# Kernel optimization log

Measured on AMD Instinct MI355X. Metric: run time of the kernel, lower is better.

Reference implementation:

```python
import jax, jax.numpy as jnp
import numpy as np

B, S = 2, 1024
ENC_IN, MARK_IN = 21, 4
PRED_LEN, C_OUT = 96, 21
E = 512                 # embedding_dim
INNER = 2 * E           # proj_factor=2.0 (library default; Model does not pass it)
NH = 8                  # mLSTM heads
DH = INNER // NH        # 128
K = 4                   # causal conv1d kernel
BS = 4                  # qkv_proj_blocksize
NHP = INNER // BS       # 256 block-diagonal proj heads
NB = 4                  # num_blocks
EPS = 1e-5


def setup_inputs() -> dict:
    key = jax.random.key(0)
    ks = jax.random.split(key, 24)
    it = iter(range(24))
    def n(shape, s=0.02):
        return jax.random.normal(ks[next(it)], shape, jnp.float32) * s
    return {
        "x_enc": n((B, S, ENC_IN), 1.0),
        "x_mark_enc": n((B, S, MARK_IN), 1.0),
        "x_dec": n((B, PRED_LEN, ENC_IN), 1.0),
        "x_mark_dec": n((B, PRED_LEN, MARK_IN), 1.0),
        "emb_W": n((ENC_IN + MARK_IN, E), 0.05),
        "emb_b": jnp.zeros((E,), jnp.float32),
        "ln_w": jnp.ones((NB, E), jnp.float32),
        "up_W": n((NB, E, 2 * INNER)),
        "conv_W": n((NB, INNER, K), 0.1),
        "conv_b": jnp.zeros((NB, INNER), jnp.float32),
        "q_W": n((NB, NHP, BS, BS), 0.1),
        "k_W": n((NB, NHP, BS, BS), 0.1),
        "v_W": n((NB, NHP, BS, BS), 0.1),
        "ig_W": n((NB, 3 * INNER, NH)),
        "ig_b": jnp.zeros((NB, NH), jnp.float32),
        "fg_W": n((NB, 3 * INNER, NH)),
        "fg_b": jnp.tile(jnp.linspace(3.0, 6.0, NH, dtype=jnp.float32), (NB, 1)),
        "skip": jnp.ones((NB, INNER), jnp.float32),
        "onorm_w": jnp.ones((NB, INNER), jnp.float32),
        "down_W": n((NB, INNER, E)),
        "post_ln_w": jnp.ones((E,), jnp.float32),
        "head_W": n((E, C_OUT), 0.05),
        "head_b": jnp.zeros((C_OUT,), jnp.float32),
    }


def _ln(x, w):
    mu = jnp.mean(x, -1, keepdims=True)
    var = jnp.var(x, -1, keepdims=True)
    return (x - mu) * jax.lax.rsqrt(var + EPS) * w


def _headwise(x, w):
    # block-diagonal LinearHeadwiseExpand: (B,S,INNER) with (NHP,BS,BS) blocks
    xh = x.reshape(x.shape[0], x.shape[1], NHP, BS)
    return jnp.einsum('bshd,hod->bsho', xh, w).reshape(x.shape)


def _block(x, lw, uW, cW, cb, qW, kW, vW, igW, igb, fgW, fgb, sk, ow, dW):
    xn = _ln(x, lw)
    up = xn @ uW                                  # (B,S,2*INNER)
    xm, z = up[..., :INNER], up[..., INNER:]
    # causal depthwise conv1d + SiLU
    xc = jax.lax.conv_general_dilated(
        xm.transpose(0, 2, 1), cW[:, None, :], (1,), [(K - 1, 0)],
        feature_group_count=INNER,
        dimension_numbers=('NCH', 'OIH', 'NCH')).transpose(0, 2, 1) + cb
    xc = jax.nn.silu(xc)
    q = _headwise(xc, qW)
    k = _headwise(xc, kW)
    v = _headwise(xm, vW)
    qkv = jnp.concatenate([q, k, v], -1)          # (B,S,3*INNER)
    ig = (qkv @ igW + igb).transpose(0, 2, 1)     # (B,NH,S)
    fg = (qkv @ fgW + fgb).transpose(0, 2, 1)
    qh = q.reshape(B, S, NH, DH).transpose(0, 2, 1, 3)
    kh = k.reshape(B, S, NH, DH).transpose(0, 2, 1, 3)
    vh = v.reshape(B, S, NH, DH).transpose(0, 2, 1, 3)
    # parallel stabilized mLSTM (exp-gated linear attention)
    log_f = jax.nn.log_sigmoid(fg)
    cs = jnp.cumsum(log_f, -1)                    # (B,NH,S)
    Mmat = cs[..., :, None] - cs[..., None, :]    # (B,NH,S,S) cumulative decay
    tri = jnp.tril(jnp.ones((S, S), bool))
    logD = jnp.where(tri, Mmat + ig[..., None, :], -jnp.inf)
    m = jnp.max(logD, -1, keepdims=True)          # row-wise stabilizer
    D = jnp.exp(logD - m)
    qk = jnp.einsum('bnsd,bntd->bnst', qh, kh) / (DH ** 0.5)
    C = qk * D
    norm = jnp.maximum(jnp.abs(jnp.sum(C, -1, keepdims=True)), jnp.exp(-m))
    h = jnp.einsum('bnst,bntd->bnsd', C / (norm + 1e-6), vh)
    # multi-head layernorm (groupnorm over DH per head), weight, no bias
    hn = (h - jnp.mean(h, -1, keepdims=True)) * jax.lax.rsqrt(jnp.var(h, -1, keepdims=True) + EPS)
    hn = hn.transpose(0, 2, 1, 3).reshape(B, S, INNER) * ow
    hs = (hn + sk * xc) * jax.nn.silu(z)          # learnable skip + output gate
    return x + hs @ dW                            # residual


def reference(x_enc, x_mark_enc, x_dec, x_mark_dec, emb_W, emb_b, ln_w, up_W,
              conv_W, conv_b, q_W, k_W, v_W, ig_W, ig_b, fg_W, fg_b, skip,
              onorm_w, down_W, post_ln_w, head_W, head_b):
    x = jnp.concatenate([x_enc, x_mark_enc], -1) @ emb_W + emb_b
    for i in range(NB):
        x = _block(x, ln_w[i], up_W[i], conv_W[i], conv_b[i], q_W[i], k_W[i],
                   v_W[i], ig_W[i], ig_b[i], fg_W[i], fg_b[i], skip[i],
                   onorm_w[i], down_W[i])
    x = _ln(x, post_ln_w)
    return x[:, -PRED_LEN:, :] @ head_W + head_b
```

## Files before the change

### kernel.cpp

```cpp
#include <hip/hip_runtime.h>
#include <hip/hip_bf16.h>

#define S_LEN 1024
#define E_DIM 512
#define INNER_D 1024
#define NHEAD 8
#define DHEAD 128

typedef unsigned short u16;
typedef unsigned int u32;
typedef __attribute__((ext_vector_type(8))) short short8;
typedef __attribute__((ext_vector_type(4))) float f32x4;

union S8 { short8 v; u16 u[8]; uint4 q; };

__device__ __forceinline__ u16 f2bf(float f) {
  u32 u = __float_as_uint(f);
  u32 r = u + 0x7FFFu + ((u >> 16) & 1u);
  return (u16)(r >> 16);
}
__device__ __forceinline__ float bf2f(u16 u) { return __uint_as_float(((u32)u) << 16); }

__device__ __forceinline__ void gload16(const u16* g, u16* l) {
  __builtin_amdgcn_global_load_lds((const __attribute__((address_space(1))) void*)g,
                                   (__attribute__((address_space(3))) void*)l, 16, 0, 0);
}

__global__ __launch_bounds__(128) void embed_kernel(
    const float* __restrict__ xe, const float* __restrict__ xm,
    const float* __restrict__ W, const float* __restrict__ bias,
    float* __restrict__ x)
{
  int row = blockIdx.x;
  int tid = threadIdx.x;
  __shared__ float in_s[25];
  if (tid < 21) in_s[tid] = xe[row * 21 + tid];
  else if (tid < 25) in_s[tid] = xm[row * 4 + tid - 21];
  __syncthreads();
#pragma unroll
  for (int rep = 0; rep < 4; rep++) {
    int e = tid + rep * 128;
    float acc = bias[e];
#pragma unroll
    for (int i = 0; i < 25; i++) acc += in_s[i] * W[i * E_DIM + e];
    x[(size_t)row * E_DIM + e] = acc;
  }
}

__global__ __launch_bounds__(256) void ln_kernel(
    const float* __restrict__ x, const float* __restrict__ w, u16* __restrict__ out)
{
  int row = blockIdx.x, tid = threadIdx.x;
  const float* xr = x + (size_t)row * E_DIM;
  float2 v = *(const float2*)(xr + tid * 2);
  float s = v.x + v.y, q = v.x * v.x + v.y * v.y;
#pragma unroll
  for (int off = 32; off; off >>= 1) { s += __shfl_xor(s, off); q += __shfl_xor(q, off); }
  __shared__ float ssum[4], ssq[4];
  int wv = tid >> 6;
  if ((tid & 63) == 0) { ssum[wv] = s; ssq[wv] = q; }
  __syncthreads();
  s = ssum[0] + ssum[1] + ssum[2] + ssum[3];
  q = ssq[0] + ssq[1] + ssq[2] + ssq[3];
  float mu = s * (1.f / E_DIM);
  float var = q * (1.f / E_DIM) - mu * mu;
  float rs = rsqrtf(var + 1e-5f);
  int e = tid * 2;
  ushort2 o;
  o.x = f2bf((v.x - mu) * rs * w[e]);
  o.y = f2bf((v.y - mu) * rs * w[e + 1]);
  *(ushort2*)(out + (size_t)row * E_DIM + e) = o;
}

__global__ __launch_bounds__(256) void lnhead_kernel(
    const float* __restrict__ x, const float* __restrict__ w,
    const float* __restrict__ hW, const float* __restrict__ hb,
    float* __restrict__ out)
{
  int ridx = blockIdx.x;
  int b = ridx / 96, r = ridx % 96;
  int row = b * S_LEN + (S_LEN - 96) + r;
  int tid = threadIdx.x;
  const float* xr = x + (size_t)row * E_DIM;
  float2 v = *(const float2*)(xr + tid * 2);
  float s = v.x + v.y, q = v.x * v.x + v.y * v.y;
#pragma unroll
  for (int off = 32; off; off >>= 1) { s += __shfl_xor(s, off); q += __shfl_xor(q, off); }
  __shared__ float ssum[4], ssq[4];
  __shared__ float lnv[512];
  __shared__ float part[8][32];
  int wv = tid >> 6;
  if ((tid & 63) == 0) { ssum[wv] = s; ssq[wv] = q; }
  __syncthreads();
  s = ssum[0] + ssum[1] + ssum[2] + ssum[3];
  q = ssq[0] + ssq[1] + ssq[2] + ssq[3];
  float mu = s * (1.f / E_DIM);
  float var = q * (1.f / E_DIM) - mu * mu;
  float rs = rsqrtf(var + 1e-5f);
  int e = tid * 2;
  lnv[e]     = (v.x - mu) * rs * w[e];
  lnv[e + 1] = (v.y - mu) * rs * w[e + 1];
  __syncthreads();
  int n = tid & 31, sl = tid >> 5;
  float p = 0.f;
  if (n < 21) {
#pragma unroll 8
    for (int kk = 0; kk < 64; kk++)
      p += lnv[sl * 64 + kk] * hW[(sl * 64 + kk) * 21 + n];
  }
  part[sl][n] = p;
  __syncthreads();
  if (tid < 21) {
    float acc = hb[tid];
#pragma unroll
    for (int j = 0; j < 8; j++) acc += part[j][tid];
    out[ridx * 21 + tid] = acc;
  }
}

__global__ __launch_bounds__(256) void transpose_bf16_all_kernel(
    const float* __restrict__ in0, u16* __restrict__ out0, int K, int N)
{
  __shared__ u16 T[64][72];
  int L = blockIdx.z;
  const float* in = in0 + (size_t)L * K * N;
  u16* out = out0 + (size_t)L * N * K;
  int k0 = blockIdx.x * 64, n0 = blockIdx.y * 64;
  int t = threadIdx.x;
  int kr = t >> 2, nseg = (t & 3) * 16;
  const float* src = in + (size_t)(k0 + kr) * N + n0 + nseg;
#pragma unroll
  for (int j = 0; j < 16; j++) T[kr][nseg + j] = f2bf(src[j]);
  __syncthreads();
  int nr = t >> 2, kseg = (t & 3) * 16;
  u32 u[8];
#pragma unroll
  for (int rr = 0; rr < 8; rr++) {
    u32 lo = T[kseg + 2 * rr][nr];
    u32 hi = T[kseg + 2 * rr + 1][nr];
    u[rr] = lo | (hi << 16);
  }
  u16* dst = out + (size_t)(n0 + nr) * K + k0 + kseg;
  uint4 w0 = {u[0], u[1], u[2], u[3]};
  uint4 w1 = {u[4], u[5], u[6], u[7]};
  *(uint4*)dst = w0;
  *(uint4*)(dst + 8) = w1;
}

__global__ __launch_bounds__(256) void vtrans_kernel(
    const u16* __restrict__ v, u16* __restrict__ vt)
{
  __shared__ u16 T[64][72];
  int r0 = blockIdx.x * 64;
  int d0 = blockIdx.y * 64;
  int t = threadIdx.x;
  int sr = t >> 2, dseg = (t & 3) * 16;
  const u16* src = v + (size_t)(r0 + sr) * INNER_D + d0 + dseg;
  S8 a0, a1;
  a0.q = *(const uint4*)src;
  a1.q = *(const uint4*)(src + 8);
#pragma unroll
  for (int j = 0; j < 8; j++) { T[sr][dseg + j] = a0.u[j]; T[sr][dseg + 8 + j] = a1.u[j]; }
  __syncthreads();
  int dr = t >> 2, sseg = (t & 3) * 16;
  u32 u[8];
#pragma unroll
  for (int rr = 0; rr < 8; rr++) {
    u32 lo = T[sseg + 2 * rr][dr];
    u32 hi = T[sseg + 2 * rr + 1][dr];
    u[rr] = lo | (hi << 16);
  }
  int b = r0 >> 10;
  u16* dst = vt + ((size_t)b * INNER_D + d0 + dr) * S_LEN + (r0 & (S_LEN - 1)) + sseg;
  uint4 w0 = {u[0], u[1], u[2], u[3]};
  uint4 w1 = {u[4], u[5], u[6], u[7]};
  *(uint4*)dst = w0;
  *(uint4*)(dst + 8) = w1;
}

__global__ __launch_bounds__(256) void gates_w_transpose_kernel(
    const float* __restrict__ igW, const float* __restrict__ fgW,
    u16* __restrict__ hi, u16* __restrict__ lo)
{
  int L = blockIdx.z;
  int n = blockIdx.y;
  int k = blockIdx.x * 256 + threadIdx.x;
  const float* W = ((n < 8) ? igW : fgW) + (size_t)L * 24576;
  float v = W[(size_t)k * 8 + (n & 7)];
  u16 h = f2bf(v);
  u16 l = f2bf(v - bf2f(h));
  size_t o = ((size_t)L * 16 + n) * 3072 + k;
  hi[o] = h;
  lo[o] = l;
}

__global__ __launch_bounds__(256) void gemm_bf16_split64(
    const u16* __restrict__ A, const u16* __restrict__ Bt,
    float* __restrict__ C0, u16* __restrict__ C1,
    int M, int N, int K, int split_col, int ldc)
{
  __shared__ u16 As0[128 * 32], As1[128 * 32];
  __shared__ u16 Bs0[128 * 32], Bs1[128 * 32];
  const int tid = threadIdx.x;
  const int row0 = blockIdx.y * 128, col0 = blockIdx.x * 128;
  const int wave = tid >> 6, lane = tid & 63;
  const int wr = wave >> 1, wc = wave & 1;
  const int lm = lane & 15, lq = lane >> 4;
  const int lr4 = lane >> 2;
  const int cg4 = (lane & 3) ^ (lr4 & 3);
  f32x4 acc[4][4] = {};
  const u16* Abase = A + (size_t)(row0 + lr4) * K + cg4 * 8;
  const u16* Bbase = Bt + (size_t)(col0 + lr4) * K + cg4 * 8;
  const int key = lm & 3;

#define STG_UP(AS, BS, K0) do { \
  _Pragma("unroll") for (int i = 0; i < 2; i++) \
    gload16(Abase + (size_t)((wave * 2 + i) * 16) * K + (K0), &AS[(wave * 2 + i) * 512]); \
  _Pragma("unroll") for (int i = 0; i < 2; i++) \
    gload16(Bbase + (size_t)((wave * 2 + i) * 16) * K + (K0), &BS[(wave * 2 + i) * 512]); \
} while (0)

#define CMP_UP(AS, BS) do { \
  short8 af[4], bfv[4]; \
  _Pragma("unroll") for (int i = 0; i < 4; i++) \
    af[i] = *(const short8*)&AS[(wr * 64 + i * 16 + lm) * 32 + ((lq ^ key) * 8)]; \
  _Pragma("unroll") for (int j = 0; j < 4; j++) \
    bfv[j] = *(const short8*)&BS[(wc * 64 + j * 16 + lm) * 32 + ((lq ^ key) * 8)]; \
  _Pragma("unroll") for (int i = 0; i < 4; i++) \
    _Pragma("unroll") for (int j = 0; j < 4; j++) \
      acc[i][j] = __builtin_amdgcn_mfma_f32_16x16x32_bf16(af[i], bfv[j], acc[i][j], 0, 0, 0); \
} while (0)

  STG_UP(As0, Bs0, 0);
  asm volatile("" ::: "memory");
  STG_UP(As1, Bs1, 32);
#pragma unroll
  for (int t = 0; t < 16; t++) {
    if (t < 15) asm volatile("s_waitcnt vmcnt(4)" ::: "memory");
    else        asm volatile("s_waitcnt vmcnt(0)" ::: "memory");
    __builtin_amdgcn_sched_barrier(0);
    __builtin_amdgcn_s_barrier();
    if (t & 1) CMP_UP(As1, Bs1); else CMP_UP(As0, Bs0);
    __builtin_amdgcn_s_barrier();
    if (t + 2 < 16) {
      if (t & 1) STG_UP(As1, Bs1, (t + 2) * 32);
      else       STG_UP(As0, Bs0, (t + 2) * 32);
    }
  }
#undef STG_UP
#undef CMP_UP

  const bool toC1 = (col0 >= split_col);
#pragma unroll
  for (int i = 0; i < 4; i++) {
#pragma unroll
    for (int j = 0; j < 4; j++) {
      int col = col0 - (toC1 ? split_col : 0) + wc * 64 + j * 16 + lm;
#pragma unroll
      for (int r = 0; r < 4; r++) {
        int row = row0 + wr * 64 + i * 16 + lq * 4 + r;
        if (toC1) C1[(size_t)row * ldc + col] = f2bf(acc[i][j][r]);
        else C0[(size_t)row * ldc + col] = acc[i][j][r];
      }
    }
  }
}

__global__ __launch_bounds__(256) void gemm_bf16_32(
    const u16* __restrict__ A, const u16* __restrict__ Bt,
    float* __restrict__ C, int M, int N, int K, int ldc)
{
  __shared__ u16 As0[64 * 64], As1[64 * 64];
  __shared__ u16 Bs0[64 * 64], Bs1[64 * 64];
  const int tid = threadIdx.x;
  const int row0 = blockIdx.y * 64, col0 = blockIdx.x * 64;
  const int wave = tid >> 6, lane = tid & 63;
  const int wr = wave >> 1, wc = wave & 1;
  const int lm = lane & 15, lq = lane >> 4;
  const int lr = lane >> 3;
  const int cg = (lane & 7) ^ lr;
  f32x4 acc[2][2] = {};
  const u16* Abase = A + (size_t)(row0 + lr) * K + cg * 8;
  const u16* Bbase = Bt + (size_t)(col0 + lr) * K + cg * 8;
  const int key = lm & 7;

#define STAGE_DN(AS, BS, K0) do { \
  _Pragma("unroll") for (int i = 0; i < 2; i++) \
    gload16(Abase + (size_t)((wave * 2 + i) * 8) * K + (K0), &AS[(wave * 2 + i) * 512]); \
  _Pragma("unroll") for (int j = 0; j < 2; j++) \
    gload16(Bbase + (size_t)((wave * 2 + j) * 8) * K + (K0), &BS[(wave * 2 + j) * 512]); \
} while (0)

#define COMPUTE_DN(AS, BS) do { \
  short8 af[2][2], bfv[2][2]; \
  _Pragma("unroll") for (int kc = 0; kc < 2; kc++) { \
    _Pragma("unroll") for (int i = 0; i < 2; i++) \
      af[kc][i] = *(const short8*)&AS[(wr * 32 + i * 16 + lm) * 64 + (((kc * 4 + lq) ^ key) * 8)]; \
    _Pragma("unroll") for (int j = 0; j < 2; j++) \
      bfv[kc][j] = *(const short8*)&BS[(wc * 32 + j * 16 + lm) * 64 + (((kc * 4 + lq) ^ key) * 8)]; \
  } \
  _Pragma("unroll") for (int kc = 0; kc < 2; kc++) \
    _Pragma("unroll") for (int i = 0; i < 2; i++) \
      _Pragma("unroll") for (int j = 0; j < 2; j++) \
        acc[i][j] = __builtin_amdgcn_mfma_f32_16x16x32_bf16(af[kc][i], bfv[kc][j], acc[i][j], 0, 0, 0); \
} while (0)

  STAGE_DN(As0, Bs0, 0);
  asm volatile("" ::: "memory");
  STAGE_DN(As1, Bs1, 64);
#pragma unroll
  for (int t = 0; t < 16; t++) {
    if (t < 15) asm volatile("s_waitcnt vmcnt(4)" ::: "memory");
    else        asm volatile("s_waitcnt vmcnt(0)" ::: "memory");
    __builtin_amdgcn_sched_barrier(0);
    __builtin_amdgcn_s_barrier();
    if (t & 1) COMPUTE_DN(As1, Bs1); else COMPUTE_DN(As0, Bs0);
    __builtin_amdgcn_s_barrier();
    if (t + 2 < 16) {
      if (t & 1) STAGE_DN(As1, Bs1, (t + 2) * 64);
      else       STAGE_DN(As0, Bs0, (t + 2) * 64);
    }
  }
#undef STAGE_DN
#undef COMPUTE_DN

#pragma unroll
  for (int i = 0; i < 2; i++) {
#pragma unroll
    for (int j = 0; j < 2; j++) {
      int col = col0 + wc * 32 + j * 16 + lm;
#pragma unroll
      for (int r = 0; r < 4; r++) {
        int row = row0 + wr * 32 + i * 16 + lq * 4 + r;
        C[(size_t)row * ldc + col] += acc[i][j][r];
      }
    }
  }
}

__global__ __launch_bounds__(256) void convqkv_kernel(
    const float* __restrict__ xm,
    const float* __restrict__ cw, const float* __restrict__ cb,
    const float* __restrict__ qw, const float* __restrict__ kw, const float* __restrict__ vw,
    float* __restrict__ xc, u16* __restrict__ q, u16* __restrict__ k, u16* __restrict__ v)
{
  int r0 = blockIdx.x * 8;
  int s0 = r0 & (S_LEN - 1);
  int g = threadIdx.x;
  int c0 = g * 4;
  const float* base = xm + (size_t)r0 * INNER_D + c0;

  float4 xv[11];
#pragma unroll
  for (int j = 0; j < 11; j++) {
    int ts = s0 - 3 + j;
    float4 t = {0.f, 0.f, 0.f, 0.f};
    if (ts >= 0) t = *(const float4*)(base + (ptrdiff_t)(j - 3) * INNER_D);
    xv[j] = t;
  }
  float cwv[4][4];
#pragma unroll
  for (int c = 0; c < 4; c++)
#pragma unroll
    for (int kk = 0; kk < 4; kk++) cwv[c][kk] = cw[(c0 + c) * 4 + kk];
  float cbv[4] = {cb[c0], cb[c0 + 1], cb[c0 + 2], cb[c0 + 3]};
  const float* qg = qw + g * 16;
  const float* kg = kw + g * 16;
  const float* vg = vw + g * 16;
  float qwv[16], kwv[16], vwv[16];
#pragma unroll
  for (int i = 0; i < 16; i++) { qwv[i] = qg[i]; kwv[i] = kg[i]; vwv[i] = vg[i]; }

#pragma unroll
  for (int i = 0; i < 8; i++) {
    float a0 = cbv[0], a1 = cbv[1], a2 = cbv[2], a3 = cbv[3];
#pragma unroll
    for (int kk = 0; kk < 4; kk++) {
      float4 xvv = xv[i + kk];
      a0 += xvv.x * cwv[0][kk];
      a1 += xvv.y * cwv[1][kk];
      a2 += xvv.z * cwv[2][kk];
      a3 += xvv.w * cwv[3][kk];
    }
    a0 = a0 / (1.f + __expf(-a0));
    a1 = a1 / (1.f + __expf(-a1));
    a2 = a2 / (1.f + __expf(-a2));
    a3 = a3 / (1.f + __expf(-a3));
    float4 accv = {a0, a1, a2, a3};
    *(float4*)(xc + (size_t)(r0 + i) * INNER_D + c0) = accv;

    float xcv[4] = {a0, a1, a2, a3};
    float xmv[4] = {xv[i + 3].x, xv[i + 3].y, xv[i + 3].z, xv[i + 3].w};
    ushort4 qs, ks, vs;
    u16* qp = (u16*)&qs; u16* kp = (u16*)&ks; u16* vp = (u16*)&vs;
#pragma unroll
    for (int o = 0; o < 4; o++) {
      float aq = 0.f, ak = 0.f, av = 0.f;
#pragma unroll
      for (int d = 0; d < 4; d++) {
        aq += xcv[d] * qwv[o * 4 + d];
        ak += xcv[d] * kwv[o * 4 + d];
        av += xmv[d] * vwv[o * 4 + d];
      }
      qp[o] = f2bf(aq); kp[o] = f2bf(ak); vp[o] = f2bf(av);
    }
    size_t off = (size_t)(r0 + i) * INNER_D + c0;
    *(ushort4*)(q + off) = qs;
    *(ushort4*)(k + off) = ks;
    *(ushort4*)(v + off) = vs;
  }
}

__global__ __launch_bounds__(256) void gates_mfma_kernel(
    const u16* __restrict__ q, const u16* __restrict__ k, const u16* __restrict__ v,
    const u16* __restrict__ whi, const u16* __restrict__ wlo,
    const float* __restrict__ igb, const float* __restrict__ fgb,
    float* __restrict__ ig, float* __restrict__ fg)
{
  const int blk = blockIdx.x;
  const int tid = threadIdx.x;
  const int wave = tid >> 6, lane = tid & 63;
  const int lm = lane & 15, lq = lane >> 4;
  const int grow = blk * 16 + lm;
  const u16* parts[3] = {q, k, v};
  f32x4 acc = {};
#pragma unroll 4
  for (int kc = 0; kc < 24; kc++) {
    int k0 = wave * 768 + kc * 32;
    int part = k0 >> 10;
    int idx = (k0 & 1023) + lq * 8;
    S8 a, bh_, bl_;
    a.q = *(const uint4*)(parts[part] + (size_t)grow * INNER_D + idx);
    bh_.q = *(const uint4*)(whi + (size_t)lm * 3072 + k0 + lq * 8);
    bl_.q = *(const uint4*)(wlo + (size_t)lm * 3072 + k0 + lq * 8);
    __builtin_amdgcn_s_setprio(1);
    acc = __builtin_amdgcn_mfma_f32_16x16x32_bf16(a.v, bh_.v, acc, 0, 0, 0);
    acc = __builtin_amdgcn_mfma_f32_16x16x32_bf16(a.v, bl_.v, acc, 0, 0, 0);
    __builtin_amdgcn_s_setprio(0);
  }
  __shared__ float red[4][16][17];
#pragma unroll
  for (int r = 0; r < 4; r++) red[wave][lq * 4 + r][lm] = acc[r];
  __syncthreads();
  if (wave == 0) {
#pragma unroll
    for (int r = 0; r < 4; r++) {
      int row = lq * 4 + r;
      float sum = red[0][row][lm] + red[1][row][lm] + red[2][row][lm] + red[3][row][lm];
      int growr = blk * 16 + row;
      int b = growr >> 10, s = growr & (S_LEN - 1);
      if (lm < 8) ig[((size_t)(b * NHEAD + lm) << 10) + s] = sum + igb[lm];
      else        fg[((size_t)(b * NHEAD + (lm - 8)) << 10) + s] = sum + fgb[lm - 8];
    }
  }
}

__global__ __launch_bounds__(1024) void scan_kernel(
    const float* __restrict__ ig, const float* __restrict__ fg,
    float* __restrict__ a, float* __restrict__ rm, float* __restrict__ enm)
{
  int bh = blockIdx.x;
  int t = threadIdx.x;
  int lane = t & 63, wv = t >> 6;
  __shared__ float sw[16];
  size_t o = ((size_t)bh << 10) + t;
  float f = fg[o];
  float lf = (f >= 0.f) ? -log1pf(__expf(-f)) : f - log1pf(__expf(f));
  float v = lf;
#pragma unroll
  for (int off = 1; off < 64; off <<= 1) {
    float u = __shfl_up(v, off);
    if (lane >= off) v += u;
  }
  if (lane == 63) sw[wv] = v;
  __syncthreads();
  float pre = 0.f;
  for (int w = 0; w < wv; w++) pre += sw[w];
  float cs = v + pre;
  float av = ig[o] - cs;
  a[o] = av;
  float m = av;
#pragma unroll
  for (int off = 1; off < 64; off <<= 1) {
    float u = __shfl_up(m, off);
    if (lane >= off) m = fmaxf(m, u);
  }
  __syncthreads();
  if (lane == 63) sw[wv] = m;
  __syncthreads();
  float pm = -3.4e38f;
  for (int w = 0; w < wv; w++) pm = fmaxf(pm, sw[w]);
  float rmx = fmaxf(m, pm);
  rm[o] = rmx;
  enm[o] = __expf(-(cs + rmx));
}

__device__ __constant__ int c_qt[24] = {7,15,14,15, 6,13,14,12,13, 5,11,12,10,11, 4, 9,10, 8, 9, 3, 8, 2, 1, 0};
__device__ __constant__ int c_k0[24] = {0, 0, 7, 8, 0, 0, 0, 6, 7, 0, 0, 0, 5, 6, 0, 0, 0, 4, 5, 0, 0, 0, 0, 0};
__device__ __constant__ int c_k1[24] = {8, 8,15,16, 7, 7, 7,13,14, 6, 6, 6,11,12, 5, 5, 5, 9,10, 4, 4, 3, 2, 1};
__device__ __constant__ int c_md[24] = {0, 1, 2, 2, 0, 1, 1, 2, 2, 0, 1, 1, 2, 2, 0, 1, 1, 2, 2, 0, 1, 0, 0, 0};

__global__ __launch_bounds__(256) void attn_mfma_kernel(
    const u16* __restrict__ qhg, const u16* __restrict__ khg, const u16* __restrict__ vtg,
    const float* __restrict__ a_arr, const float* __restrict__ rm_arr, const float* __restrict__ enm_arr,
    const float* __restrict__ xc, const u16* __restrict__ zh,
    const float* __restrict__ skip, const float* __restrict__ onw,
    u16* __restrict__ hs, float* __restrict__ hpart, float* __restrict__ scpart)
{
  const int bh = blockIdx.x;
  const int job = blockIdx.y;
  const int qt = c_qt[job], k0t = c_k0[job], k1t = c_k1[job], mode = c_md[job];
  const int b = bh >> 3, h = bh & 7;
  const int s0 = qt * 64;
  const int tid = threadIdx.x;
  const int wave = tid >> 6, lane = tid & 63;
  const int lm = lane & 15, lq = lane >> 4;
  const size_t rowbase = (size_t)b * S_LEN;
  const int c0 = h * DHEAD;

  __shared__ u16 Ks0[64 * 128], Ks1[64 * 128];
  __shared__ u16 Vt0[128 * 64], Vt1[128 * 64];
  __shared__ u16 Ws[64 * 72];

  short8 aq[4];
  {
    const u16* qp = qhg + (rowbase + s0 + wave * 16 + lm) * INNER_D + c0 + lq * 8;
#pragma unroll
    for (int kc = 0; kc < 4; kc++) {
      S8 tmp; tmp.q = *(const uint4*)(qp + kc * 32);
      aq[kc] = tmp.v;
    }
  }
  float rmv[4];
#pragma unroll
  for (int r = 0; r < 4; r++)
    rmv[r] = rm_arr[(size_t)bh * S_LEN + s0 + wave * 16 + lq * 4 + r];

  f32x4 accH[8] = {};
  float sc_acc[4] = {0.f, 0.f, 0.f, 0.f};
  const float scale = 0.08838834764831845f;
  const int lr16 = lane >> 4;
  const int ls16 = lane & 15;
  const int lr8 = lane >> 3;
  const int cgv = (lane & 7) ^ lr8;
  const u16* vtbase = vtg + ((size_t)b * INNER_D + c0) * S_LEN;

  float ae0[4], ae1[4];

#define PREF(KS, VS, AE, T0) do { \
  _Pragma("unroll") for (int j = 0; j < 4; j++) { \
    int rK = (wave * 4 + j) * 4 + lr16; \
    int cgk = ls16 ^ (rK & 7); \
    gload16(khg + (rowbase + (T0) + rK) * INNER_D + c0 + cgk * 8, &KS[(wave * 4 + j) * 512]); \
  } \
  _Pragma("unroll") for (int j = 0; j < 4; j++) { \
    int rV = (wave * 4 + j) * 8 + lr8; \
    gload16(vtbase + (size_t)rV * S_LEN + (T0) + cgv * 8, &VS[(wave * 4 + j) * 512]); \
  } \
  _Pragma("unroll") for (int cb = 0; cb < 4; cb++) \
    AE[cb] = a_arr[(size_t)bh * S_LEN + (T0) + cb * 16 + lm]; \
} while (0)

#define QK_STEP(KS, PACC) do { \
  __builtin_amdgcn_s_setprio(1); \
  _Pragma("unroll") for (int kc = 0; kc < 4; kc++) \
    _Pragma("unroll") for (int cb = 0; cb < 4; cb++) { \
      short8 bk = *(const short8*)&KS[(cb * 16 + lm) * 128 + (((kc * 4 + lq) ^ (lm & 7)) * 8)]; \
      PACC[cb] = __builtin_amdgcn_mfma_f32_16x16x32_bf16(aq[kc], bk, PACC[cb], 0, 0, 0); \
    } \
  __builtin_amdgcn_s_setprio(0); \
} while (0)

#define W_PV(AE, VT, T0, PACC) do { \
  float wpart[4] = {0.f, 0.f, 0.f, 0.f}; \
  _Pragma("unroll") for (int cb = 0; cb < 4; cb++) { \
    int colg = (T0) + cb * 16 + lm; \
    float ea = AE[cb]; \
    _Pragma("unroll") for (int r = 0; r < 4; r++) { \
      int rowg = s0 + wave * 16 + lq * 4 + r; \
      float wv = PACC[cb][r] * scale * __expf(ea - rmv[r]); \
      if (colg > rowg) wv = 0.f; \
      wpart[r] += wv; \
      Ws[(wave * 16 + lq * 4 + r) * 72 + cb * 16 + lm] = f2bf(wv); \
    } \
  } \
  _Pragma("unroll") for (int r = 0; r < 4; r++) { \
    float sr = wpart[r]; \
    sr += __shfl_xor(sr, 1); sr += __shfl_xor(sr, 2); \
    sr += __shfl_xor(sr, 4); sr += __shfl_xor(sr, 8); \
    sc_acc[r] += sr; \
  } \
  __builtin_amdgcn_s_setprio(1); \
  _Pragma("unroll") for (int kc = 0; kc < 2; kc++) { \
    short8 aw = *(const short8*)&Ws[(wave * 16 + lm) * 72 + kc * 32 + lq * 8]; \
    _Pragma("unroll") for (int nb = 0; nb < 8; nb++) { \
      short8 bv = *(const short8*)&VT[(nb * 16 + lm) * 64 + (((kc * 4 + lq) ^ (lm & 7)) * 8)]; \
      accH[nb] = __builtin_amdgcn_mfma_f32_16x16x32_bf16(aw, bv, accH[nb], 0, 0, 0); \
    } \
  } \
  __builtin_amdgcn_s_setprio(0); \
} while (0)

  int kt = k0t;
  PREF(Ks0, Vt0, ae0, kt * 64);
  asm volatile("" ::: "memory");
  if (kt + 1 < k1t) PREF(Ks1, Vt1, ae1, (kt + 1) * 64);

  while (true) {
    {
      if (kt + 1 < k1t) asm volatile("s_waitcnt vmcnt(12)" ::: "memory");
      else              asm volatile("s_waitcnt vmcnt(0)" ::: "memory");
      __builtin_amdgcn_sched_barrier(0);
      __builtin_amdgcn_s_barrier();
      f32x4 pacc[4] = {};
      QK_STEP(Ks0, pacc);
      W_PV(ae0, Vt0, kt * 64, pacc);
      __builtin_amdgcn_s_barrier();
      if (kt + 2 < k1t) PREF(Ks0, Vt0, ae0, (kt + 2) * 64);
      kt++;
      if (kt >= k1t) break;
    }
    {
      if (kt + 1 < k1t) asm volatile("s_waitcnt vmcnt(12)" ::: "memory");
      else              asm volatile("s_waitcnt vmcnt(0)" ::: "memory");
      __builtin_amdgcn_sched_barrier(0);
      __builtin_amdgcn_s_barrier();
      f32x4 pacc[4] = {};
      QK_STEP(Ks1, pacc);
      W_PV(ae1, Vt1, kt * 64, pacc);
      __builtin_amdgcn_s_barrier();
      if (kt + 2 < k1t) PREF(Ks1, Vt1, ae1, (kt + 2) * 64);
      kt++;
      if (kt >= k1t) break;
    }
  }
#undef PREF
#undef QK_STEP
#undef W_PV

  if (mode != 0) {
    int slot = mode - 1;
    int qr = qt - 8;
    float* Hp = hpart + (((size_t)slot * 16 + bh) * 8 + qr) * 8192;
    float* sp = scpart + ((slot * 16 + bh) * 8 + qr) * 64;
#pragma unroll
    for (int r = 0; r < 4; r++) {
      int row = wave * 16 + lq * 4 + r;
      if (lm == 0) sp[row] = sc_acc[r];
#pragma unroll
      for (int nb = 0; nb < 8; nb++)
        Hp[row * 128 + nb * 16 + lm] = accH[nb][r];
    }
    return;
  }

  float inv[4], muv[4], rsv[4];
#pragma unroll
  for (int r = 0; r < 4; r++) {
    int rowg = s0 + wave * 16 + lq * 4 + r;
    float nrm = fmaxf(fabsf(sc_acc[r]), enm_arr[(size_t)bh * S_LEN + rowg]);
    inv[r] = 1.f / (nrm + 1e-6f);
  }
#pragma unroll
  for (int r = 0; r < 4; r++) {
    float s = 0.f, qq = 0.f;
#pragma unroll
    for (int nb = 0; nb < 8; nb++) {
      float hv = accH[nb][r] * inv[r];
      accH[nb][r] = hv;
      s += hv; qq += hv * hv;
    }
    s += __shfl_xor(s, 1); s += __shfl_xor(s, 2); s += __shfl_xor(s, 4); s += __shfl_xor(s, 8);
    qq += __shfl_xor(qq, 1); qq += __shfl_xor(qq, 2); qq += __shfl_xor(qq, 4); qq += __shfl_xor(qq, 8);
    float mu = s * (1.f / DHEAD);
    float var = qq * (1.f / DHEAD) - mu * mu;
    muv[r] = mu;
    rsv[r] = rsqrtf(var + 1e-5f);
  }
  float ow[8], sk[8];
#pragma unroll
  for (int nb = 0; nb < 8; nb++) {
    ow[nb] = onw[c0 + nb * 16 + lm];
    sk[nb] = skip[c0 + nb * 16 + lm];
  }
#pragma unroll
  for (int r = 0; r < 4; r++) {
    int rowg = s0 + wave * 16 + lq * 4 + r;
    size_t base = (rowbase + rowg) * INNER_D + c0;
#pragma unroll
    for (int nb = 0; nb < 8; nb++) {
      int d = nb * 16 + lm;
      float xcv = xc[base + d];
      float zv = bf2f(zh[base + d]);
      float hn = (accH[nb][r] - muv[r]) * rsv[r] * ow[nb] + sk[nb] * xcv;
      float o = hn * (zv / (1.f + __expf(-zv)));
      hs[base + d] = f2bf(o);
    }
  }
}

__global__ __launch_bounds__(256) void attn_combine_kernel(
    const float* __restrict__ hpart, const float* __restrict__ scpart,
    const float* __restrict__ enm,
    const float* __restrict__ xc, const u16* __restrict__ zh,
    const float* __restrict__ skip, const float* __restrict__ onw,
    u16* __restrict__ hs)
{
  int wave = threadIdx.x >> 6, lane = threadIdx.x & 63;
  int gid = blockIdx.x * 4 + wave;
  int bh = gid >> 9;
  int rr = gid & 511;
  int qr = rr >> 6, row = rr & 63;
  int b = bh >> 3, hh = bh & 7;
  int s = (qr + 8) * 64 + row;
  size_t off = (((size_t)bh) * 8 + qr) * 8192 + row * 128 + lane * 2;
  float2 h0 = *(const float2*)(hpart + off);
  float2 h1 = *(const float2*)(hpart + 1048576 + off);
  int sidx = (bh * 8 + qr) * 64 + row;
  float sc = scpart[sidx] + scpart[8192 + sidx];
  float nrm = fmaxf(fabsf(sc), enm[(size_t)bh * S_LEN + s]);
  float inv = 1.f / (nrm + 1e-6f);
  float hx = (h0.x + h1.x) * inv, hy = (h0.y + h1.y) * inv;
  float sm = hx + hy, sq = hx * hx + hy * hy;
#pragma unroll
  for (int off2 = 32; off2; off2 >>= 1) { sm += __shfl_xor(sm, off2); sq += __shfl_xor(sq, off2); }
  float mu = sm * (1.f / DHEAD);
  float var = sq * (1.f / DHEAD) - mu * mu;
  float rs = rsqrtf(var + 1e-5f);
  int c0 = hh * DHEAD + lane * 2;
  size_t base = ((size_t)(b * S_LEN + s)) * INNER_D + c0;
  float2 xc2 = *(const float2*)(xc + base);
  ushort2 z2u = *(const ushort2*)(zh + base);
  float z2x = bf2f(z2u.x), z2y = bf2f(z2u.y);
  float skx = skip[c0], sky = skip[c0 + 1];
  float owx = onw[c0],  owy = onw[c0 + 1];
  ushort2 o;
  o.x = f2bf(((hx - mu) * rs * owx + skx * xc2.x) * (z2x / (1.f + __expf(-z2x))));
  o.y = f2bf(((hy - mu) * rs * owy + sky * xc2.y) * (z2y / (1.f + __expf(-z2y))));
  *(ushort2*)(hs + base) = o;
}

extern "C" void kernel_launch(void* const* d_in, const int* in_sizes, int n_in,
                              void* d_out, int out_size, void* d_ws, size_t ws_size,
                              hipStream_t stream)
{
  const float* x_enc   = (const float*)d_in[0];
  const float* x_mark  = (const float*)d_in[1];
  const float* emb_W   = (const float*)d_in[4];
  const float* emb_b   = (const float*)d_in[5];
  const float* ln_w    = (const float*)d_in[6];
  const float* up_W    = (const float*)d_in[7];
  const float* conv_W  = (const float*)d_in[8];
  const float* conv_b  = (const float*)d_in[9];
  const float* q_W     = (const float*)d_in[10];
  const float* k_W     = (const float*)d_in[11];
  const float* v_W     = (const float*)d_in[12];
  const float* ig_W    = (const float*)d_in[13];
  const float* ig_b    = (const float*)d_in[14];
  const float* fg_W    = (const float*)d_in[15];
  const float* fg_b    = (const float*)d_in[16];
  const float* skip_w  = (const float*)d_in[17];
  const float* onorm_w = (const float*)d_in[18];
  const float* down_W  = (const float*)d_in[19];
  const float* post_ln = (const float*)d_in[20];
  const float* head_W  = (const float*)d_in[21];
  const float* head_b  = (const float*)d_in[22];

  float* p = (float*)d_ws;
  float* x    = p; p += 1048576;
  float* xm   = p; p += 2097152;
  float* xc   = p; p += 2097152;
  float* igb_ = p; p += 16384;
  float* fgb_ = p; p += 16384;
  float* ab   = p; p += 16384;
  float* rmb  = p; p += 16384;
  float* enmb = p; p += 16384;
  float* ln96 = p; p += 98304;
  u16* qhb = (u16*)p; p += 1048576;
  u16* khb = (u16*)p; p += 1048576;
  u16* vhb = (u16*)p; p += 1048576;
  u16* zh  = (u16*)p; p += 524288;
  u16* xnh = (u16*)p; p += 524288;
  u16* upWtA = (u16*)p; p += 2097152;
  u16* dnWtA = (u16*)p; p += 1048576;
  u16* gtwH = (u16*)p; p += 98304;
  u16* gtwL = (u16*)p; p += 98304;
  float* hpart = p; p += 2097152;
  float* scpart = p; p += 16384;
  u16* vtg = (u16*)p; p += 1048576;
  u16* hsbh = (u16*)xm;

  embed_kernel<<<2048, 128, 0, stream>>>(x_enc, x_mark, emb_W, emb_b, x);
  transpose_bf16_all_kernel<<<dim3(8, 32, 4), 256, 0, stream>>>(up_W, upWtA, 512, 2048);
  transpose_bf16_all_kernel<<<dim3(16, 8, 4), 256, 0, stream>>>(down_W, dnWtA, 1024, 512);
  gates_w_transpose_kernel<<<dim3(12, 16, 4), 256, 0, stream>>>(ig_W, fg_W, gtwH, gtwL);

  for (int L = 0; L < 4; L++) {
    ln_kernel<<<2048, 256, 0, stream>>>(x, ln_w + L * 512, xnh);
    gemm_bf16_split64<<<dim3(16, 16), 256, 0, stream>>>(
        xnh, upWtA + (size_t)L * 1048576, xm, zh, 2048, 2048, 512, 1024, 1024);
    convqkv_kernel<<<256, 256, 0, stream>>>(
        xm, conv_W + L * 4096, conv_b + L * 1024,
        q_W + L * 4096, k_W + L * 4096, v_W + L * 4096,
        xc, qhb, khb, vhb);
    vtrans_kernel<<<dim3(32, 16), 256, 0, stream>>>(vhb, vtg);
    gates_mfma_kernel<<<128, 256, 0, stream>>>(
        qhb, khb, vhb, gtwH + (size_t)L * 49152, gtwL + (size_t)L * 49152,
        ig_b + L * 8, fg_b + L * 8, igb_, fgb_);
    scan_kernel<<<16, 1024, 0, stream>>>(igb_, fgb_, ab, rmb, enmb);
    attn_mfma_kernel<<<dim3(16, 24), 256, 0, stream>>>(
        qhb, khb, vtg, ab, rmb, enmb, xc, zh,
        skip_w + L * 1024, onorm_w + L * 1024, hsbh, hpart, scpart);
    attn_combine_kernel<<<2048, 256, 0, stream>>>(
        hpart, scpart, enmb, xc, zh, skip_w + L * 1024, onorm_w + L * 1024, hsbh);
    gemm_bf16_32<<<dim3(8, 32), 256, 0, stream>>>(
        hsbh, dnWtA + (size_t)L * 524288, x, 2048, 512, 1024, 512);
  }

  lnhead_kernel<<<192, 256, 0, stream>>>(x, post_ln, head_W, head_b, (float*)d_out);
}
```

Before: 464.7 us.

## Fuse prep kernels, write V-transpose in convqkv, triple-buffer GEMM staging

The embedding, weight-transpose and gate-weight split kernels are merged into one launch with a block-index dispatch, saving three launches. The convqkv kernel now also writes the transposed V directly, so the per-layer vtrans kernel and its extra read of V are gone. Both bf16 GEMMs go from double to triple-buffered LDS staging with deeper vmcnt waits to hide more global-load latency. The cost is more LDS per block, which may lower occupancy, and narrower 16-byte scattered writes for V transpose.

New measurement: 454.4 us. 2.2% less time.

```diff
diff --git a/kernel.cpp b/kernel.cpp
--- a/kernel.cpp
+++ b/kernel.cpp
@@ -26,24 +26,79 @@
                                    (__attribute__((address_space(3))) void*)l, 16, 0, 0);
 }
 
-__global__ __launch_bounds__(128) void embed_kernel(
-    const float* __restrict__ xe, const float* __restrict__ xm,
-    const float* __restrict__ W, const float* __restrict__ bias,
+__device__ __forceinline__ void prep_transpose(
+    const float* __restrict__ in, u16* __restrict__ out, int K, int N,
+    int k0, int n0, int t, u16 (*T)[72])
+{
+  int kr = t >> 2, nseg = (t & 3) * 16;
+  const float* src = in + (size_t)(k0 + kr) * N + n0 + nseg;
+#pragma unroll
+  for (int j = 0; j < 16; j++) T[kr][nseg + j] = f2bf(src[j]);
+  __syncthreads();
+  int nr = t >> 2, kseg = (t & 3) * 16;
+  u32 u[8];
+#pragma unroll
+  for (int rr = 0; rr < 8; rr++) {
+    u32 lo = T[kseg + 2 * rr][nr];
+    u32 hi = T[kseg + 2 * rr + 1][nr];
+    u[rr] = lo | (hi << 16);
+  }
+  u16* dst = out + (size_t)(n0 + nr) * K + k0 + kseg;
+  uint4 w0 = {u[0], u[1], u[2], u[3]};
+  uint4 w1 = {u[4], u[5], u[6], u[7]};
+  *(uint4*)dst = w0;
+  *(uint4*)(dst + 8) = w1;
+}
+
+__global__ __launch_bounds__(256) void prep_kernel(
+    const float* __restrict__ up_W, u16* __restrict__ upWt,
+    const float* __restrict__ down_W, u16* __restrict__ dnWt,
+    const float* __restrict__ igW, const float* __restrict__ fgW,
+    u16* __restrict__ ghi, u16* __restrict__ glo,
+    const float* __restrict__ xe, const float* __restrict__ xmk,
+    const float* __restrict__ eW, const float* __restrict__ eb,
     float* __restrict__ x)
 {
-  int row = blockIdx.x;
-  int tid = threadIdx.x;
+  __shared__ u16 T[64][72];
   __shared__ float in_s[25];
-  if (tid < 21) in_s[tid] = xe[row * 21 + tid];
-  else if (tid < 25) in_s[tid] = xm[row * 4 + tid - 21];
-  __syncthreads();
-#pragma unroll
-  for (int rep = 0; rep < 4; rep++) {
-    int e = tid + rep * 128;
-    float acc = bias[e];
-#pragma unroll
-    for (int i = 0; i < 25; i++) acc += in_s[i] * W[i * E_DIM + e];
-    x[(size_t)row * E_DIM + e] = acc;
+  int id = blockIdx.x;
+  int t = threadIdx.x;
+  if (id < 1024) {
+    int bx = id & 7, rest = id >> 3;
+    int by = rest & 31, L = rest >> 5;
+    prep_transpose(up_W + (size_t)L * 512 * 2048, upWt + (size_t)L * 1048576,
+                   512, 2048, bx * 64, by * 64, t, T);
+  } else if (id < 1536) {
+    int id2 = id - 1024;
+    int bx = id2 & 15, rest = id2 >> 4;
+    int by = rest & 7, L = rest >> 3;
+    prep_transpose(down_W + (size_t)L * 1024 * 512, dnWt + (size_t)L * 524288,
+                   1024, 512, bx * 64, by * 64, t, T);
+  } else if (id < 2304) {
+    int id3 = id - 1536;
+    int bx = id3 % 12, rest = id3 / 12;
+    int n = rest & 15, L = rest >> 4;
+    int k = bx * 256 + t;
+    const float* W = ((n < 8) ? igW : fgW) + (size_t)L * 24576;
+    float v = W[(size_t)k * 8 + (n & 7)];
+    u16 h = f2bf(v);
+    u16 l = f2bf(v - bf2f(h));
+    size_t o = ((size_t)L * 16 + n) * 3072 + k;
+    ghi[o] = h;
+    glo[o] = l;
+  } else {
+    int row = id - 2304;
+    if (t < 21) in_s[t] = xe[row * 21 + t];
+    else if (t < 25) in_s[t] = xmk[row * 4 + t - 21];
+    __syncthreads();
+#pragma unroll
+    for (int rep = 0; rep < 2; rep++) {
+      int e = t + rep * 256;
+      float acc = eb[e];
+#pragma unroll
+      for (int i = 0; i < 25; i++) acc += in_s[i] * eW[i * E_DIM + e];
+      x[(size_t)row * E_DIM + e] = acc;
+    }
   }
 }
 
@@ -118,89 +173,13 @@
   }
 }
 
-__global__ __launch_bounds__(256) void transpose_bf16_all_kernel(
-    const float* __restrict__ in0, u16* __restrict__ out0, int K, int N)
-{
-  __shared__ u16 T[64][72];
-  int L = blockIdx.z;
-  const float* in = in0 + (size_t)L * K * N;
-  u16* out = out0 + (size_t)L * N * K;
-  int k0 = blockIdx.x * 64, n0 = blockIdx.y * 64;
-  int t = threadIdx.x;
-  int kr = t >> 2, nseg = (t & 3) * 16;
-  const float* src = in + (size_t)(k0 + kr) * N + n0 + nseg;
-#pragma unroll
-  for (int j = 0; j < 16; j++) T[kr][nseg + j] = f2bf(src[j]);
-  __syncthreads();
-  int nr = t >> 2, kseg = (t & 3) * 16;
-  u32 u[8];
-#pragma unroll
-  for (int rr = 0; rr < 8; rr++) {
-    u32 lo = T[kseg + 2 * rr][nr];
-    u32 hi = T[kseg + 2 * rr + 1][nr];
-    u[rr] = lo | (hi << 16);
-  }
-  u16* dst = out + (size_t)(n0 + nr) * K + k0 + kseg;
-  uint4 w0 = {u[0], u[1], u[2], u[3]};
-  uint4 w1 = {u[4], u[5], u[6], u[7]};
-  *(uint4*)dst = w0;
-  *(uint4*)(dst + 8) = w1;
-}
-
-__global__ __launch_bounds__(256) void vtrans_kernel(
-    const u16* __restrict__ v, u16* __restrict__ vt)
-{
-  __shared__ u16 T[64][72];
-  int r0 = blockIdx.x * 64;
-  int d0 = blockIdx.y * 64;
-  int t = threadIdx.x;
-  int sr = t >> 2, dseg = (t & 3) * 16;
-  const u16* src = v + (size_t)(r0 + sr) * INNER_D + d0 + dseg;
-  S8 a0, a1;
-  a0.q = *(const uint4*)src;
-  a1.q = *(const uint4*)(src + 8);
-#pragma unroll
-  for (int j = 0; j < 8; j++) { T[sr][dseg + j] = a0.u[j]; T[sr][dseg + 8 + j] = a1.u[j]; }
-  __syncthreads();
-  int dr = t >> 2, sseg = (t & 3) * 16;
-  u32 u[8];
-#pragma unroll
-  for (int rr = 0; rr < 8; rr++) {
-    u32 lo = T[sseg + 2 * rr][dr];
-    u32 hi = T[sseg + 2 * rr + 1][dr];
-    u[rr] = lo | (hi << 16);
-  }
-  int b = r0 >> 10;
-  u16* dst = vt + ((size_t)b * INNER_D + d0 + dr) * S_LEN + (r0 & (S_LEN - 1)) + sseg;
-  uint4 w0 = {u[0], u[1], u[2], u[3]};
-  uint4 w1 = {u[4], u[5], u[6], u[7]};
-  *(uint4*)dst = w0;
-  *(uint4*)(dst + 8) = w1;
-}
-
-__global__ __launch_bounds__(256) void gates_w_transpose_kernel(
-    const float* __restrict__ igW, const float* __restrict__ fgW,
-    u16* __restrict__ hi, u16* __restrict__ lo)
-{
-  int L = blockIdx.z;
-  int n = blockIdx.y;
-  int k = blockIdx.x * 256 + threadIdx.x;
-  const float* W = ((n < 8) ? igW : fgW) + (size_t)L * 24576;
-  float v = W[(size_t)k * 8 + (n & 7)];
-  u16 h = f2bf(v);
-  u16 l = f2bf(v - bf2f(h));
-  size_t o = ((size_t)L * 16 + n) * 3072 + k;
-  hi[o] = h;
-  lo[o] = l;
-}
-
 __global__ __launch_bounds__(256) void gemm_bf16_split64(
     const u16* __restrict__ A, const u16* __restrict__ Bt,
     float* __restrict__ C0, u16* __restrict__ C1,
     int M, int N, int K, int split_col, int ldc)
 {
-  __shared__ u16 As0[128 * 32], As1[128 * 32];
-  __shared__ u16 Bs0[128 * 32], Bs1[128 * 32];
+  __shared__ u16 As0[128 * 32], As1[128 * 32], As2[128 * 32];
+  __shared__ u16 Bs0[128 * 32], Bs1[128 * 32], Bs2[128 * 32];
   const int tid = threadIdx.x;
   const int row0 = blockIdx.y * 128, col0 = blockIdx.x * 128;
   const int wave = tid >> 6, lane = tid & 63;
@@ -234,17 +213,23 @@
   STG_UP(As0, Bs0, 0);
   asm volatile("" ::: "memory");
   STG_UP(As1, Bs1, 32);
+  asm volatile("" ::: "memory");
+  STG_UP(As2, Bs2, 64);
 #pragma unroll
   for (int t = 0; t < 16; t++) {
-    if (t < 15) asm volatile("s_waitcnt vmcnt(4)" ::: "memory");
-    else        asm volatile("s_waitcnt vmcnt(0)" ::: "memory");
+    if (t <= 13)      asm volatile("s_waitcnt vmcnt(8)" ::: "memory");
+    else if (t == 14) asm volatile("s_waitcnt vmcnt(4)" ::: "memory");
+    else              asm volatile("s_waitcnt vmcnt(0)" ::: "memory");
     __builtin_amdgcn_sched_barrier(0);
     __builtin_amdgcn_s_barrier();
-    if (t & 1) CMP_UP(As1, Bs1); else CMP_UP(As0, Bs0);
+    if ((t % 3) == 0)      CMP_UP(As0, Bs0);
+    else if ((t % 3) == 1) CMP_UP(As1, Bs1);
+    else                   CMP_UP(As2, Bs2);
     __builtin_amdgcn_s_barrier();
-    if (t + 2 < 16) {
-      if (t & 1) STG_UP(As1, Bs1, (t + 2) * 32);
-      else       STG_UP(As0, Bs0, (t + 2) * 32);
+    if (t + 3 < 16) {
+      if ((t % 3) == 0)      STG_UP(As0, Bs0, (t + 3) * 32);
+      else if ((t % 3) == 1) STG_UP(As1, Bs1, (t + 3) * 32);
+      else                   STG_UP(As2, Bs2, (t + 3) * 32);
     }
   }
 #undef STG_UP
@@ -270,8 +255,8 @@
     const u16* __restrict__ A, const u16* __restrict__ Bt,
     float* __restrict__ C, int M, int N, int K, int ldc)
 {
-  __shared__ u16 As0[64 * 64], As1[64 * 64];
-  __shared__ u16 Bs0[64 * 64], Bs1[64 * 64];
+  __shared__ u16 As0[64 * 64], As1[64 * 64], As2[64 * 64];
+  __shared__ u16 Bs0[64 * 64], Bs1[64 * 64], Bs2[64 * 64];
   const int tid = threadIdx.x;
   const int row0 = blockIdx.y * 64, col0 = blockIdx.x * 64;
   const int wave = tid >> 6, lane = tid & 63;
@@ -308,17 +293,23 @@
   STAGE_DN(As0, Bs0, 0);
   asm volatile("" ::: "memory");
   STAGE_DN(As1, Bs1, 64);
+  asm volatile("" ::: "memory");
+  STAGE_DN(As2, Bs2, 128);
 #pragma unroll
   for (int t = 0; t < 16; t++) {
-    if (t < 15) asm volatile("s_waitcnt vmcnt(4)" ::: "memory");
-    else        asm volatile("s_waitcnt vmcnt(0)" ::: "memory");
+    if (t <= 13)      asm volatile("s_waitcnt vmcnt(8)" ::: "memory");
+    else if (t == 14) asm volatile("s_waitcnt vmcnt(4)" ::: "memory");
+    else              asm volatile("s_waitcnt vmcnt(0)" ::: "memory");
     __builtin_amdgcn_sched_barrier(0);
     __builtin_amdgcn_s_barrier();
-    if (t & 1) COMPUTE_DN(As1, Bs1); else COMPUTE_DN(As0, Bs0);
+    if ((t % 3) == 0)      COMPUTE_DN(As0, Bs0);
+    else if ((t % 3) == 1) COMPUTE_DN(As1, Bs1);
+    else                   COMPUTE_DN(As2, Bs2);
     __builtin_amdgcn_s_barrier();
-    if (t + 2 < 16) {
-      if (t & 1) STAGE_DN(As1, Bs1, (t + 2) * 64);
-      else       STAGE_DN(As0, Bs0, (t + 2) * 64);
+    if (t + 3 < 16) {
+      if ((t % 3) == 0)      STAGE_DN(As0, Bs0, (t + 3) * 64);
+      else if ((t % 3) == 1) STAGE_DN(As1, Bs1, (t + 3) * 64);
+      else                   STAGE_DN(As2, Bs2, (t + 3) * 64);
     }
   }
 #undef STAGE_DN
@@ -342,7 +333,8 @@
     const float* __restrict__ xm,
     const float* __restrict__ cw, const float* __restrict__ cb,
     const float* __restrict__ qw, const float* __restrict__ kw, const float* __restrict__ vw,
-    float* __restrict__ xc, u16* __restrict__ q, u16* __restrict__ k, u16* __restrict__ v)
+    float* __restrict__ xc, u16* __restrict__ q, u16* __restrict__ k, u16* __restrict__ v,
+    u16* __restrict__ vt)
 {
   int r0 = blockIdx.x * 8;
   int s0 = r0 & (S_LEN - 1);
@@ -371,6 +363,8 @@
 #pragma unroll
   for (int i = 0; i < 16; i++) { qwv[i] = qg[i]; kwv[i] = kg[i]; vwv[i] = vg[i]; }
 
+  u32 vt_pack[4][4];
+
 #pragma unroll
   for (int i = 0; i < 8; i++) {
     float a0 = cbv[0], a1 = cbv[1], a2 = cbv[2], a3 = cbv[3];
@@ -402,12 +396,22 @@
         ak += xcv[d] * kwv[o * 4 + d];
         av += xmv[d] * vwv[o * 4 + d];
       }
-      qp[o] = f2bf(aq); kp[o] = f2bf(ak); vp[o] = f2bf(av);
+      qp[o] = f2bf(aq); kp[o] = f2bf(ak);
+      u16 vv = f2bf(av);
+      vp[o] = vv;
+      if ((i & 1) == 0) vt_pack[o][i >> 1] = (u32)vv;
+      else              vt_pack[o][i >> 1] |= ((u32)vv) << 16;
     }
     size_t off = (size_t)(r0 + i) * INNER_D + c0;
     *(ushort4*)(q + off) = qs;
     *(ushort4*)(k + off) = ks;
     *(ushort4*)(v + off) = vs;
+  }
+  u16* vtb = vt + ((size_t)((r0 >> 10) * INNER_D + c0)) * S_LEN + s0;
+#pragma unroll
+  for (int c = 0; c < 4; c++) {
+    uint4 wv4 = {vt_pack[c][0], vt_pack[c][1], vt_pack[c][2], vt_pack[c][3]};
+    *(uint4*)(vtb + (size_t)c * S_LEN) = wv4;
   }
 }
 
@@ -790,10 +794,9 @@
   u16* vtg = (u16*)p; p += 1048576;
   u16* hsbh = (u16*)xm;
 
-  embed_kernel<<<2048, 128, 0, stream>>>(x_enc, x_mark, emb_W, emb_b, x);
-  transpose_bf16_all_kernel<<<dim3(8, 32, 4), 256, 0, stream>>>(up_W, upWtA, 512, 2048);
-  transpose_bf16_all_kernel<<<dim3(16, 8, 4), 256, 0, stream>>>(down_W, dnWtA, 1024, 512);
-  gates_w_transpose_kernel<<<dim3(12, 16, 4), 256, 0, stream>>>(ig_W, fg_W, gtwH, gtwL);
+  prep_kernel<<<4352, 256, 0, stream>>>(
+      up_W, upWtA, down_W, dnWtA, ig_W, fg_W, gtwH, gtwL,
+      x_enc, x_mark, emb_W, emb_b, x);
 
   for (int L = 0; L < 4; L++) {
     ln_kernel<<<2048, 256, 0, stream>>>(x, ln_w + L * 512, xnh);
@@ -802,8 +805,7 @@
     convqkv_kernel<<<256, 256, 0, stream>>>(
         xm, conv_W + L * 4096, conv_b + L * 1024,
         q_W + L * 4096, k_W + L * 4096, v_W + L * 4096,
-        xc, qhb, khb, vhb);
-    vtrans_kernel<<<dim3(32, 16), 256, 0, stream>>>(vhb, vtg);
+        xc, qhb, khb, vhb, vtg);
     gates_mfma_kernel<<<128, 256, 0, stream>>>(
         qhb, khb, vhb, gtwH + (size_t)L * 49152, gtwL + (size_t)L * 49152,
         ig_b + L * 8, fg_b + L * 8, igb_, fgb_);
```
